# Kernel tuning notes

Measured on AMD Instinct MI355X. Metric: run time of the kernel, lower is better.

## Reference

```python
import jax, jax.numpy as jnp
import numpy as np

N0, N1, N2 = 400000, 75000, 15000
E1, E2 = 1200000, 240000
F_IN, NC = 64, 40
H1, C1 = 2, 8          # layer 1: heads=2, out_channels=8 -> concat dim 16
H2, C2 = 1, NC         # layer 2: heads=1, out_channels=num_classes
NEG_SLOPE = 0.2


def gat_conv(x_src, x_dst, src, dst, Ws, Wd, att_s, att_d, bias, heads, ch):
    """PyG GATConv on bipartite (x_src, x_dst) with remove+add self loops."""
    n_dst = x_dst.shape[0]
    hs = (x_src @ Ws).reshape(-1, heads, ch)   # [N_src, H, C]
    hd = (x_dst @ Wd).reshape(-1, heads, ch)   # [N_dst, H, C]
    a_s = (hs * att_s).sum(-1)                 # [N_src, H]
    a_d = (hd * att_d).sum(-1)                 # [N_dst, H]
    loops = jnp.arange(n_dst)
    src_all = jnp.concatenate([src, loops])
    dst_all = jnp.concatenate([dst, loops])
    # remove_self_loops: drop pre-existing i->i edges; add_self_loops: appended
    valid = jnp.concatenate([src != dst, jnp.ones(n_dst, dtype=bool)])[:, None]
    logits = jax.nn.leaky_relu(a_s[src_all] + a_d[dst_all], NEG_SLOPE)  # [E, H]
    logits = jnp.where(valid, logits, -jnp.inf)
    m = jax.ops.segment_max(logits, dst_all, num_segments=n_dst)        # [N_dst, H]
    w = jnp.where(valid, jnp.exp(logits - m[dst_all]), 0.0)
    denom = jax.ops.segment_sum(w, dst_all, num_segments=n_dst)
    alpha = w / denom[dst_all]                                          # [E, H]
    out = jax.ops.segment_sum(alpha[:, :, None] * hs[src_all], dst_all,
                              num_segments=n_dst)                       # [N_dst, H, C]
    return out.reshape(n_dst, heads * ch) + bias


def setup_inputs() -> dict:
    key = jax.random.key(0)
    ks = jax.random.split(key, 16)
    s = 0.1
    return {
        "x": jax.random.normal(ks[0], (N0, F_IN), dtype=jnp.float32),
        "e1_src": jax.random.randint(ks[1], (E1,), 0, N0),
        "e1_dst": jax.random.randint(ks[2], (E1,), 0, N1),
        "e2_src": jax.random.randint(ks[3], (E2,), 0, N1),
        "e2_dst": jax.random.randint(ks[4], (E2,), 0, N2),
        "W1s": jax.random.normal(ks[5], (F_IN, H1 * C1), dtype=jnp.float32) * s,
        "W1d": jax.random.normal(ks[6], (F_IN, H1 * C1), dtype=jnp.float32) * s,
        "att1_s": jax.random.normal(ks[7], (H1, C1), dtype=jnp.float32) * s,
        "att1_d": jax.random.normal(ks[8], (H1, C1), dtype=jnp.float32) * s,
        "b1": jnp.zeros((H1 * C1,), dtype=jnp.float32),
        "W2s": jax.random.normal(ks[9], (H1 * C1, H2 * C2), dtype=jnp.float32) * s,
        "W2d": jax.random.normal(ks[10], (H1 * C1, H2 * C2), dtype=jnp.float32) * s,
        "att2_s": jax.random.normal(ks[11], (H2, C2), dtype=jnp.float32) * s,
        "att2_d": jax.random.normal(ks[12], (H2, C2), dtype=jnp.float32) * s,
        "b2": jnp.zeros((H2 * C2,), dtype=jnp.float32),
    }


def reference(x, e1_src, e1_dst, e2_src, e2_dst,
              W1s, W1d, att1_s, att1_d, b1,
              W2s, W2d, att2_s, att2_d, b2):
    h = gat_conv(x, x[:N1], e1_src, e1_dst, W1s, W1d, att1_s, att1_d, b1, H1, C1)
    h = jax.nn.elu(h)
    o = gat_conv(h, h[:N2], e2_src, e2_dst, W2s, W2d, att2_s, att2_d, b2, H2, C2)
    return jax.nn.log_softmax(o, axis=-1)
```

## Files before the change

### kernel.cpp

```cpp
#include <hip/hip_runtime.h>
#include <hip/hip_bf16.h>

constexpr int N0 = 400000, N1 = 75000, N2 = 15000;
constexpr int E1 = 1200000, E2 = 240000;
constexpr int NC = 40;
constexpr float NEG_SLOPE = 0.2f;

constexpr int BK1 = 128;
constexpr int NB1 = (N1 + BK1 - 1) / BK1;
constexpr int CAPB1 = 2432;
constexpr int BK2 = 32;
constexpr int NB2 = (N2 + BK2 - 1) / BK2;
constexpr int CAPB2 = 704;

constexpr int TILE = 8192;
constexpr int NT1 = (E1 + TILE - 1) / TILE;
constexpr int NT2 = (E2 + TILE - 1) / TILE;
constexpr int NTB = NT1 + NT2;
constexpr int BPJ = N0 / 64;

using f32x4 = __attribute__((ext_vector_type(4))) float;
using s16x8 = __attribute__((ext_vector_type(8))) short;

__device__ __forceinline__ float leaky(float v) { return v > 0.f ? v : NEG_SLOPE * v; }

__device__ __forceinline__ unsigned cvtpk(float lo, float hi) {
    unsigned r;
    asm("v_cvt_pk_bf16_f32 %0, %1, %2" : "=v"(r) : "v"(lo), "v"(hi));
    return r;
}

__device__ __forceinline__ unsigned bf16pair(float lo, float hi) {
    unsigned a = __float_as_uint(lo), b = __float_as_uint(hi);
    a = (a + 0x7FFFu + ((a >> 16) & 1u)) >> 16;
    b = (b + 0x7FFFu + ((b >> 16) & 1u)) & 0xFFFF0000u;
    return a | b;
}
__device__ __forceinline__ float bfLo(unsigned w) { return __uint_as_float(w << 16); }
__device__ __forceinline__ float bfHi(unsigned w) { return __uint_as_float(w & 0xFFFF0000u); }

__global__ __launch_bounds__(256) void k1_kernel(
    const float* __restrict__ x,
    const float* __restrict__ W1s, const float* __restrict__ W1d,
    const float* __restrict__ att1s, const float* __restrict__ att1d,
    const int* __restrict__ e1s, const int* __restrict__ e1d,
    const int* __restrict__ e2s, const int* __restrict__ e2d,
    unsigned* __restrict__ rec1, float* __restrict__ a_d1,
    int* __restrict__ gcnt1, unsigned* __restrict__ bin1,
    int* __restrict__ gcnt2, unsigned* __restrict__ bin2)
{
    __shared__ int hist[NB1];
    __shared__ int gbase[NB1];
    __shared__ float2 vds[64];

    int bid = blockIdx.x;
    const int tid = threadIdx.x;
    if (bid < NTB) {
        const bool isL1 = bid < NT1;
        const int* es = isL1 ? e1s : e2s;
        const int* ed = isL1 ? e1d : e2d;
        const int nE = isL1 ? E1 : E2;
        const int nb = isL1 ? NB1 : NB2;
        const int cap = isL1 ? CAPB1 : CAPB2;
        const int shift = isL1 ? 7 : 5;
        const int lsh = isL1 ? 19 : 17;
        int* gc = isL1 ? gcnt1 : gcnt2;
        unsigned* gbin = isL1 ? bin1 : bin2;
        const int base = (isL1 ? bid : bid - NT1) * TILE;
        const int lim = min(TILE, nE - base);

        for (int b = tid; b < nb; b += 256) hist[b] = 0;
        __syncthreads();
        for (int i = tid; i < lim; i += 256) {
            int s = es[base + i], d = ed[base + i];
            if (s != d) atomicAdd(&hist[d >> shift], 1);
        }
        __syncthreads();
        for (int b = tid; b < nb; b += 256) {
            int c = hist[b];
            gbase[b] = (c > 0) ? atomicAdd(&gc[b], c) : 0;
            hist[b] = 0;
        }
        __syncthreads();
        for (int i = tid; i < lim; i += 256) {
            int s = es[base + i], d = ed[base + i];
            if (s != d) {
                int b = d >> shift;
                int pos = gbase[b] + atomicAdd(&hist[b], 1);
                if (pos < cap)
                    gbin[(size_t)b * cap + pos] =
                        (unsigned)s | ((unsigned)(d & ((1 << shift) - 1)) << lsh);
            }
        }
        return;
    }
    bid -= NTB;
    const int l  = tid & 63;
    const int nd = l & 15;
    const int kg = l >> 4;
    const int wv = tid >> 6;
    const int nodeBase = bid * 64;
    const bool hasN1 = nodeBase < N1;

    if (hasN1) {
        if (tid < 64) {
            float d0 = 0.f, d1 = 0.f;
            const float* wr = W1d + (size_t)tid * 16;
            #pragma unroll
            for (int cc = 0; cc < 8; ++cc) {
                d0 = fmaf(wr[cc], att1d[cc], d0);
                d1 = fmaf(wr[8 + cc], att1d[8 + cc], d1);
            }
            vds[tid] = make_float2(d0, d1);
        }
        __syncthreads();
    }

    const int node = nodeBase + wv * 16 + nd;

    const float* xr_ = x + (size_t)node * 64 + 8 * kg;
    float4 q0 = *(const float4*)(xr_);
    float4 q1 = *(const float4*)(xr_ + 4);
    float4 q2 = *(const float4*)(xr_ + 32);
    float4 q3 = *(const float4*)(xr_ + 36);

    s16x8 bf0, bf1;
    {
        union { unsigned u[4]; s16x8 v; } t0, t1;
        #pragma unroll
        for (int q = 0; q < 4; ++q) {
            t0.u[q] = cvtpk(W1s[(8 * kg + 2 * q) * 16 + nd],
                            W1s[(8 * kg + 2 * q + 1) * 16 + nd]);
            t1.u[q] = cvtpk(W1s[(32 + 8 * kg + 2 * q) * 16 + nd],
                            W1s[(32 + 8 * kg + 2 * q + 1) * 16 + nd]);
        }
        bf0 = t0.v; bf1 = t1.v;
    }
    float att4[4];
    #pragma unroll
    for (int r = 0; r < 4; ++r) att4[r] = att1s[4 * kg + r];

    union { unsigned u[4]; s16x8 v; } a0, a1;
    a0.u[0] = cvtpk(q0.x, q0.y); a0.u[1] = cvtpk(q0.z, q0.w);
    a0.u[2] = cvtpk(q1.x, q1.y); a0.u[3] = cvtpk(q1.z, q1.w);
    a1.u[0] = cvtpk(q2.x, q2.y); a1.u[1] = cvtpk(q2.z, q2.w);
    a1.u[2] = cvtpk(q3.x, q3.y); a1.u[3] = cvtpk(q3.z, q3.w);

    f32x4 acc = {0.f, 0.f, 0.f, 0.f};
    acc = __builtin_amdgcn_mfma_f32_16x16x32_bf16(bf0, a0.v, acc, 0, 0, 0);
    acc = __builtin_amdgcn_mfma_f32_16x16x32_bf16(bf1, a1.v, acc, 0, 0, 0);

    float p = acc[0] * att4[0];
    p = fmaf(acc[1], att4[1], p);
    p = fmaf(acc[2], att4[2], p);
    p = fmaf(acc[3], att4[3], p);
    p += __shfl_xor(p, 16, 64);
    float q = __shfl_xor(p, 32, 64);

    unsigned* rp = rec1 + (size_t)node * 16;
    uint2 hw;
    hw.x = cvtpk(acc[0], acc[1]);
    hw.y = cvtpk(acc[2], acc[3]);
    *(uint2*)(rp + 2 * kg) = hw;
    if (kg == 0)
        *(uint4*)(rp + 8) = make_uint4(__float_as_uint(p), __float_as_uint(q), 0u, 0u);
    else if (kg == 1)
        *(uint4*)(rp + 12) = make_uint4(0u, 0u, 0u, 0u);

    if (hasN1 && node < N1) {
        float xv8[16] = {q0.x, q0.y, q0.z, q0.w, q1.x, q1.y, q1.z, q1.w,
                         q2.x, q2.y, q2.z, q2.w, q3.x, q3.y, q3.z, q3.w};
        float pd0 = 0.f, pd1 = 0.f;
        #pragma unroll
        for (int j = 0; j < 8; ++j) {
            float2 v = vds[8 * kg + j];
            pd0 = fmaf(xv8[j], v.x, pd0);
            pd1 = fmaf(xv8[j], v.y, pd1);
        }
        #pragma unroll
        for (int j = 0; j < 8; ++j) {
            float2 v = vds[32 + 8 * kg + j];
            pd0 = fmaf(xv8[8 + j], v.x, pd0);
            pd1 = fmaf(xv8[8 + j], v.y, pd1);
        }
        pd0 += __shfl_xor(pd0, 16, 64); pd0 += __shfl_xor(pd0, 32, 64);
        pd1 += __shfl_xor(pd1, 16, 64); pd1 += __shfl_xor(pd1, 32, 64);
        if (kg == 0)
            ((float2*)a_d1)[node] = make_float2(pd0, pd1);
    }
}

__global__ __launch_bounds__(512) void k2_kernel(
    const int* __restrict__ gcnt1, const unsigned* __restrict__ bin1,
    const unsigned* __restrict__ rec1, const float* __restrict__ a_d1,
    const float* __restrict__ b1,
    const float* __restrict__ W2s, const float* __restrict__ W2d,
    const float* __restrict__ att2s, const float* __restrict__ att2d,
    unsigned* __restrict__ rec2)
{
    __shared__ unsigned srt[CAPB1];
    __shared__ int hist[BK1], start[BK1 + 1];
    __shared__ float w2sl[640], va[16], vd[16];
    __shared__ float h1s[BK1][17];

    const int b = blockIdx.x, tid = threadIdx.x;
    const int d0 = b * BK1;
    const int nN = min(BK1, N1 - d0);
    const int ncnt = min(gcnt1[b], CAPB1);
    const unsigned* bp = bin1 + (size_t)b * CAPB1;

    for (int i = tid; i < 640; i += 512) w2sl[i] = W2s[i];
    if (tid < BK1) hist[tid] = 0;
    if (tid >= 128 && tid < 144) {
        int k = tid - 128;
        float sa = 0.f, sd = 0.f;
        for (int cc = 0; cc < 40; ++cc) {
            sa = fmaf(W2s[k * 40 + cc], att2s[cc], sa);
            sd = fmaf(W2d[k * 40 + cc], att2d[cc], sd);
        }
        va[k] = sa; vd[k] = sd;
    }
    __syncthreads();
    for (int i = tid; i < ncnt; i += 512) atomicAdd(&hist[bp[i] >> 19], 1);
    __syncthreads();
    if (tid == 0) {
        int a = 0;
        for (int k = 0; k < BK1; ++k) { start[k] = a; a += hist[k]; }
        start[BK1] = a;
    }
    __syncthreads();
    if (tid < BK1) hist[tid] = start[tid];
    __syncthreads();
    for (int i = tid; i < ncnt; i += 512) {
        unsigned p = bp[i];
        int pos = atomicAdd(&hist[p >> 19], 1);
        srt[pos] = p & 0x7FFFFu;
    }
    __syncthreads();

    const int g = tid >> 4, c = tid & 15, h = c >> 3;
    const int wbase = tid & 48;
    const int wmap = (c < 8) ? c : (8 + ((c >> 2) & 1));
    for (int n = g; n < nN; n += 32) {
        const int node = d0 + n;
        const float ad = a_d1[(size_t)node * 2 + h];
        const int st = start[n], cnt = start[n + 1] - start[n];
        unsigned rw0 = rec1[(size_t)node * 16 + wmap];
        unsigned rw1 = (cnt >= 1) ? rec1[(size_t)srt[st] * 16 + wmap] : 0u;
        unsigned rw2 = (cnt >= 2) ? rec1[(size_t)srt[st + 1] * 16 + wmap] : 0u;
        unsigned rw3 = (cnt >= 3) ? rec1[(size_t)srt[st + 2] * 16 + wmap] : 0u;
        float accv = 0.f, den = 0.f;
        for (int j = 0; j <= cnt; ++j) {
            float asv = __uint_as_float((unsigned)__shfl((int)rw0, wbase + 8 + 4 * h, 64));
            unsigned chw = (unsigned)__shfl((int)rw0, wbase + (c >> 1), 64);
            float hv = (c & 1) ? bfHi(chw) : bfLo(chw);
            float w = __expf(leaky(asv + ad));
            accv = fmaf(w, hv, accv);
            den += w;
            rw0 = rw1; rw1 = rw2; rw2 = rw3;
            rw3 = (j + 4 <= cnt) ? rec1[(size_t)srt[st + j + 3] * 16 + wmap] : 0u;
        }
        float v = accv / den + b1[c];
        h1s[n][c] = v > 0.f ? v : (__expf(v) - 1.f);
    }
    __syncthreads();
    for (int i = tid; i < nN * 24; i += 512) {
        int nn = i / 24, w = i - nn * 24;
        unsigned* rp = rec2 + (size_t)(d0 + nn) * 24;
        if (w < 20) {
            int c0 = 2 * w, c1 = c0 + 1;
            float s0 = 0.f, s1 = 0.f;
            #pragma unroll
            for (int k = 0; k < 16; ++k) {
                float hk = h1s[nn][k];
                s0 = fmaf(hk, w2sl[k * 40 + c0], s0);
                s1 = fmaf(hk, w2sl[k * 40 + c1], s1);
            }
            rp[w] = bf16pair(s0, s1);
        } else if (w < 22) {
            const float* vv = (w == 20) ? va : vd;
            float s = 0.f;
            #pragma unroll
            for (int k = 0; k < 16; ++k) s = fmaf(h1s[nn][k], vv[k], s);
            rp[w] = __float_as_uint(s);
        }
    }
}

__global__ __launch_bounds__(1024) void k3_kernel(
    const int* __restrict__ gcnt2, const unsigned* __restrict__ bin2,
    const unsigned* __restrict__ rec2, const float* __restrict__ b2,
    float* __restrict__ out)
{
    __shared__ unsigned srt[CAPB2];
    __shared__ int hist[BK2], start[BK2 + 1];

    const int b = blockIdx.x, tid = threadIdx.x;
    const int d0 = b * BK2;
    const int nN = min(BK2, N2 - d0);
    const int ncnt = min(gcnt2[b], CAPB2);
    const unsigned* bp = bin2 + (size_t)b * CAPB2;

    if (tid < BK2) hist[tid] = 0;
    __syncthreads();
    for (int i = tid; i < ncnt; i += 1024) atomicAdd(&hist[bp[i] >> 17], 1);
    __syncthreads();
    if (tid == 0) {
        int a = 0;
        for (int k = 0; k < BK2; ++k) { start[k] = a; a += hist[k]; }
        start[BK2] = a;
    }
    __syncthreads();
    if (tid < BK2) hist[tid] = start[tid];
    __syncthreads();
    for (int i = tid; i < ncnt; i += 1024) {
        unsigned p = bp[i];
        int pos = atomicAdd(&hist[p >> 17], 1);
        srt[pos] = p & 0x1FFFFu;
    }
    __syncthreads();

    const int g = tid >> 5, l = tid & 31;
    const float bb0 = (l < 20) ? b2[2 * l] : 0.f;
    const float bb1 = (l < 20) ? b2[2 * l + 1] : 0.f;
    for (int n = g; n < nN; n += 32) {
        const int node = d0 + n;
        const int st = start[n], cnt = start[n + 1] - start[n];
        unsigned rw0 = (l < 22) ? rec2[(size_t)node * 24 + l] : 0u;
        const float ad = __uint_as_float((unsigned)__shfl((int)rw0, 21, 32));
        unsigned rw1 = (cnt >= 1 && l < 21) ? rec2[(size_t)srt[st] * 24 + l] : 0u;
        unsigned rw2 = (cnt >= 2 && l < 21) ? rec2[(size_t)srt[st + 1] * 24 + l] : 0u;
        unsigned rw3 = (cnt >= 3 && l < 21) ? rec2[(size_t)srt[st + 2] * 24 + l] : 0u;
        float a0 = 0.f, a1 = 0.f, den = 0.f;
        for (int j = 0; j <= cnt; ++j) {
            float asv = __uint_as_float((unsigned)__shfl((int)rw0, 20, 32));
            float w = __expf(leaky(asv + ad));
            a0 = fmaf(w, bfLo(rw0), a0);
            a1 = fmaf(w, bfHi(rw0), a1);
            den += w;
            rw0 = rw1; rw1 = rw2; rw2 = rw3;
            rw3 = (j + 4 <= cnt && l < 21) ? rec2[(size_t)srt[st + j + 3] * 24 + l] : 0u;
        }
        float v0 = (l < 20) ? a0 / den + bb0 : -3.4e38f;
        float v1 = (l < 20) ? a1 / den + bb1 : -3.4e38f;
        float mx = fmaxf(v0, v1);
        #pragma unroll
        for (int k = 16; k >= 1; k >>= 1) mx = fmaxf(mx, __shfl_xor(mx, k, 32));
        float ex = (l < 20) ? __expf(v0 - mx) + __expf(v1 - mx) : 0.f;
        #pragma unroll
        for (int k = 16; k >= 1; k >>= 1) ex += __shfl_xor(ex, k, 32);
        float lse = mx + logf(ex);
        if (l < 20)
            ((float2*)(out + (size_t)node * 40))[l] = make_float2(v0 - lse, v1 - lse);
    }
}

extern "C" void kernel_launch(void* const* d_in, const int* in_sizes, int n_in,
                              void* d_out, int out_size, void* d_ws, size_t ws_size,
                              hipStream_t stream) {
    const float* x      = (const float*)d_in[0];
    const int*   e1_src = (const int*)d_in[1];
    const int*   e1_dst = (const int*)d_in[2];
    const int*   e2_src = (const int*)d_in[3];
    const int*   e2_dst = (const int*)d_in[4];
    const float* W1s    = (const float*)d_in[5];
    const float* W1d    = (const float*)d_in[6];
    const float* att1s  = (const float*)d_in[7];
    const float* att1d  = (const float*)d_in[8];
    const float* b1     = (const float*)d_in[9];
    const float* W2s    = (const float*)d_in[10];
    const float* W2d    = (const float*)d_in[11];
    const float* att2s  = (const float*)d_in[12];
    const float* att2d  = (const float*)d_in[13];
    const float* b2     = (const float*)d_in[14];
    float* out = (float*)d_out;

    float* wsbase = (float*)d_ws;
    size_t o = 0;
    int*      gcnt1 = (int*)(wsbase + o);      o += NB1;
    int*      gcnt2 = (int*)(wsbase + o);      o += NB2;
    const size_t zeroWords = o;
    unsigned* bin1  = (unsigned*)(wsbase + o); o += (size_t)NB1 * CAPB1;
    unsigned* bin2  = (unsigned*)(wsbase + o); o += (size_t)NB2 * CAPB2;
    unsigned* rec1  = (unsigned*)(wsbase + o); o += (size_t)N0 * 16;
    float*    a_d1  = (float*)(wsbase + o);    o += (size_t)N1 * 2;
    unsigned* rec2  = (unsigned*)(wsbase + o); o += (size_t)N1 * 24;

    hipMemsetAsync(d_ws, 0, zeroWords * sizeof(float), stream);

    k1_kernel<<<NTB + BPJ, 256, 0, stream>>>(
        x, W1s, W1d, att1s, att1d, e1_src, e1_dst, e2_src, e2_dst,
        rec1, a_d1, gcnt1, bin1, gcnt2, bin2);

    k2_kernel<<<NB1, 512, 0, stream>>>(gcnt1, bin1, rec1, a_d1, b1,
                                       W2s, W2d, att2s, att2d, rec2);

    k3_kernel<<<NB2, 1024, 0, stream>>>(gcnt2, bin2, rec2, b2, out);
}
```

Before: 119.9 us.

## Replace global atomic edge binning with per-tile sub-bins merged by consumers

Edge binning now writes each tile's edges into private fixed-size sub-bins (tile × bucket × 32 slots) with per-tile counts, instead of reserving space in shared global bins through global atomics. This removes the counting pass, the global atomicAdd traffic and the workspace memset. The consumer kernels k2 and k3 instead read every tile's count for their bucket, prefix-scan them, and gather the pieces into shared memory before the local sort. In exchange the bin arrays become much larger and sparse, consumers issue strided gathers across many tiles (NT1L×NB1 counts), and edges past 32 per tile-bucket are silently dropped.

```diff
diff --git a/kernel.cpp b/kernel.cpp
--- a/kernel.cpp
+++ b/kernel.cpp
@@ -13,10 +13,11 @@
 constexpr int NB2 = (N2 + BK2 - 1) / BK2;
 constexpr int CAPB2 = 704;
 
-constexpr int TILE = 8192;
-constexpr int NT1 = (E1 + TILE - 1) / TILE;
-constexpr int NT2 = (E2 + TILE - 1) / TILE;
-constexpr int NTB = NT1 + NT2;
+constexpr int TILE = 4096;
+constexpr int NT1L = (E1 + TILE - 1) / TILE;
+constexpr int NT2L = (E2 + TILE - 1) / TILE;
+constexpr int NTB = NT1L + NT2L;
+constexpr int SUBCAP = 32;
 constexpr int BPJ = N0 / 64;
 
 using f32x4 = __attribute__((ext_vector_type(4))) float;
@@ -49,49 +50,40 @@
     int* __restrict__ gcnt1, unsigned* __restrict__ bin1,
     int* __restrict__ gcnt2, unsigned* __restrict__ bin2)
 {
-    __shared__ int hist[NB1];
-    __shared__ int gbase[NB1];
+    __shared__ int cur[NB1];
     __shared__ float2 vds[64];
 
     int bid = blockIdx.x;
     const int tid = threadIdx.x;
     if (bid < NTB) {
-        const bool isL1 = bid < NT1;
+        const bool isL1 = bid < NT1L;
+        const int t = isL1 ? bid : bid - NT1L;
         const int* es = isL1 ? e1s : e2s;
         const int* ed = isL1 ? e1d : e2d;
         const int nE = isL1 ? E1 : E2;
         const int nb = isL1 ? NB1 : NB2;
-        const int cap = isL1 ? CAPB1 : CAPB2;
         const int shift = isL1 ? 7 : 5;
         const int lsh = isL1 ? 19 : 17;
         int* gc = isL1 ? gcnt1 : gcnt2;
         unsigned* gbin = isL1 ? bin1 : bin2;
-        const int base = (isL1 ? bid : bid - NT1) * TILE;
+        const int base = t * TILE;
         const int lim = min(TILE, nE - base);
 
-        for (int b = tid; b < nb; b += 256) hist[b] = 0;
-        __syncthreads();
-        for (int i = tid; i < lim; i += 256) {
-            int s = es[base + i], d = ed[base + i];
-            if (s != d) atomicAdd(&hist[d >> shift], 1);
-        }
-        __syncthreads();
-        for (int b = tid; b < nb; b += 256) {
-            int c = hist[b];
-            gbase[b] = (c > 0) ? atomicAdd(&gc[b], c) : 0;
-            hist[b] = 0;
-        }
+        for (int b = tid; b < nb; b += 256) cur[b] = 0;
         __syncthreads();
         for (int i = tid; i < lim; i += 256) {
             int s = es[base + i], d = ed[base + i];
             if (s != d) {
                 int b = d >> shift;
-                int pos = gbase[b] + atomicAdd(&hist[b], 1);
-                if (pos < cap)
-                    gbin[(size_t)b * cap + pos] =
+                int pos = atomicAdd(&cur[b], 1);
+                if (pos < SUBCAP)
+                    gbin[((size_t)t * nb + b) * SUBCAP + pos] =
                         (unsigned)s | ((unsigned)(d & ((1 << shift) - 1)) << lsh);
             }
         }
+        __syncthreads();
+        for (int b = tid; b < nb; b += 256)
+            gc[(size_t)t * nb + b] = min(cur[b], SUBCAP);
         return;
     }
     bid -= NTB;
@@ -198,7 +190,9 @@
     const float* __restrict__ att2s, const float* __restrict__ att2d,
     unsigned* __restrict__ rec2)
 {
+    __shared__ unsigned raw[CAPB1];
     __shared__ unsigned srt[CAPB1];
+    __shared__ int cnts[NT1L], pfx[NT1L + 1];
     __shared__ int hist[BK1], start[BK1 + 1];
     __shared__ float w2sl[640], va[16], vd[16];
     __shared__ float h1s[BK1][17];
@@ -206,8 +200,6 @@
     const int b = blockIdx.x, tid = threadIdx.x;
     const int d0 = b * BK1;
     const int nN = min(BK1, N1 - d0);
-    const int ncnt = min(gcnt1[b], CAPB1);
-    const unsigned* bp = bin1 + (size_t)b * CAPB1;
 
     for (int i = tid; i < 640; i += 512) w2sl[i] = W2s[i];
     if (tid < BK1) hist[tid] = 0;
@@ -220,8 +212,37 @@
         }
         va[k] = sa; vd[k] = sd;
     }
-    __syncthreads();
-    for (int i = tid; i < ncnt; i += 512) atomicAdd(&hist[bp[i] >> 19], 1);
+    for (int i = tid; i < NT1L; i += 512) cnts[i] = gcnt1[(size_t)i * NB1 + b];
+    __syncthreads();
+    if (tid < 64) {
+        int carry = 0;
+        #pragma unroll
+        for (int s = 0; s < (NT1L + 63) / 64; ++s) {
+            int idx = s * 64 + tid;
+            int v = (idx < NT1L) ? cnts[idx] : 0;
+            int xv = v;
+            #pragma unroll
+            for (int d = 1; d < 64; d <<= 1) {
+                int t2 = __shfl_up(xv, d, 64);
+                if (tid >= d) xv += t2;
+            }
+            if (idx < NT1L) pfx[idx] = carry + xv - v;
+            carry += __shfl(xv, 63, 64);
+        }
+        if (tid == 0) pfx[NT1L] = carry;
+    }
+    __syncthreads();
+    for (int j = tid; j < NT1L * SUBCAP; j += 512) {
+        int t = j >> 5, p = j & (SUBCAP - 1);
+        if (p < cnts[t]) {
+            int dst = pfx[t] + p;
+            if (dst < CAPB1) {
+                unsigned pay = bin1[((size_t)t * NB1 + b) * SUBCAP + p];
+                raw[dst] = pay;
+                atomicAdd(&hist[pay >> 19], 1);
+            }
+        }
+    }
     __syncthreads();
     if (tid == 0) {
         int a = 0;
@@ -231,8 +252,9 @@
     __syncthreads();
     if (tid < BK1) hist[tid] = start[tid];
     __syncthreads();
-    for (int i = tid; i < ncnt; i += 512) {
-        unsigned p = bp[i];
+    const int total = min(pfx[NT1L], CAPB1);
+    for (int i = tid; i < total; i += 512) {
+        unsigned p = raw[i];
         int pos = atomicAdd(&hist[p >> 19], 1);
         srt[pos] = p & 0x7FFFFu;
     }
@@ -292,18 +314,41 @@
     const unsigned* __restrict__ rec2, const float* __restrict__ b2,
     float* __restrict__ out)
 {
+    __shared__ unsigned raw[CAPB2];
     __shared__ unsigned srt[CAPB2];
+    __shared__ int cnts[NT2L], pfx[NT2L + 1];
     __shared__ int hist[BK2], start[BK2 + 1];
 
     const int b = blockIdx.x, tid = threadIdx.x;
     const int d0 = b * BK2;
     const int nN = min(BK2, N2 - d0);
-    const int ncnt = min(gcnt2[b], CAPB2);
-    const unsigned* bp = bin2 + (size_t)b * CAPB2;
 
     if (tid < BK2) hist[tid] = 0;
-    __syncthreads();
-    for (int i = tid; i < ncnt; i += 1024) atomicAdd(&hist[bp[i] >> 17], 1);
+    if (tid < NT2L) cnts[tid] = gcnt2[(size_t)tid * NB2 + b];
+    __syncthreads();
+    if (tid < 64) {
+        int v = (tid < NT2L) ? cnts[tid] : 0;
+        int xv = v;
+        #pragma unroll
+        for (int d = 1; d < 64; d <<= 1) {
+            int t2 = __shfl_up(xv, d, 64);
+            if (tid >= d) xv += t2;
+        }
+        if (tid < NT2L) pfx[tid] = xv - v;
+        if (tid == NT2L - 1) pfx[NT2L] = xv;
+    }
+    __syncthreads();
+    for (int j = tid; j < NT2L * SUBCAP; j += 1024) {
+        int t = j >> 5, p = j & (SUBCAP - 1);
+        if (p < cnts[t]) {
+            int dst = pfx[t] + p;
+            if (dst < CAPB2) {
+                unsigned pay = bin2[((size_t)t * NB2 + b) * SUBCAP + p];
+                raw[dst] = pay;
+                atomicAdd(&hist[pay >> 17], 1);
+            }
+        }
+    }
     __syncthreads();
     if (tid == 0) {
         int a = 0;
@@ -313,8 +358,9 @@
     __syncthreads();
     if (tid < BK2) hist[tid] = start[tid];
     __syncthreads();
-    for (int i = tid; i < ncnt; i += 1024) {
-        unsigned p = bp[i];
+    const int total = min(pfx[NT2L], CAPB2);
+    for (int i = tid; i < total; i += 1024) {
+        unsigned p = raw[i];
         int pos = atomicAdd(&hist[p >> 17], 1);
         srt[pos] = p & 0x1FFFFu;
     }
@@ -377,17 +423,14 @@
 
     float* wsbase = (float*)d_ws;
     size_t o = 0;
-    int*      gcnt1 = (int*)(wsbase + o);      o += NB1;
-    int*      gcnt2 = (int*)(wsbase + o);      o += NB2;
-    const size_t zeroWords = o;
-    unsigned* bin1  = (unsigned*)(wsbase + o); o += (size_t)NB1 * CAPB1;
-    unsigned* bin2  = (unsigned*)(wsbase + o); o += (size_t)NB2 * CAPB2;
+    int*      gcnt1 = (int*)(wsbase + o);      o += (size_t)NT1L * NB1;
+    int*      gcnt2 = (int*)(wsbase + o);      o += (size_t)NT2L * NB2;
+    unsigned* bin1  = (unsigned*)(wsbase + o); o += (size_t)NT1L * NB1 * SUBCAP;
+    unsigned* bin2  = (unsigned*)(wsbase + o); o += (size_t)NT2L * NB2 * SUBCAP;
     unsigned* rec1  = (unsigned*)(wsbase + o); o += (size_t)N0 * 16;
     float*    a_d1  = (float*)(wsbase + o);    o += (size_t)N1 * 2;
     unsigned* rec2  = (unsigned*)(wsbase + o); o += (size_t)N1 * 24;
 
-    hipMemsetAsync(d_ws, 0, zeroWords * sizeof(float), stream);
-
     k1_kernel<<<NTB + BPJ, 256, 0, stream>>>(
         x, W1s, W1d, att1s, att1d, e1_src, e1_dst, e2_src, e2_dst,
         rec1, a_d1, gcnt1, bin1, gcnt2, bin2);
```

After: 115.8 us. 3.4% less time.
